# Kernel tuning notes

Hardware: AMD Instinct MI355X
Metric: run time of the kernel (lower is better)

Reference implementation:

```python
import jax, jax.numpy as jnp
import numpy as np

N, E, IN_DIM, C = 30000, 300000, 128, 16


def _xavier(key, shape):
    fan_in, fan_out = shape[1], shape[0]
    lim = np.sqrt(6.0 / (fan_in + fan_out))
    return jax.random.uniform(key, shape, jnp.float32, -lim, lim)


def layernorm(x, g, b, eps=1e-5):
    mu = jnp.mean(x, axis=-1, keepdims=True)
    var = jnp.var(x, axis=-1, keepdims=True)
    return (x - mu) * jax.lax.rsqrt(var + eps) * g + b


def setup_inputs() -> dict:
    key = jax.random.key(0)
    ks = jax.random.split(key, 8)
    D9 = C * 9            # 144
    DI = C * (C * 2)      # 512
    return {
        "x": jax.random.normal(ks[0], (N, IN_DIM), jnp.float32),
        "h": jax.random.normal(ks[1], (N, IN_DIM), jnp.float32),
        "local_frames": jax.random.normal(ks[2], (N, 3, 3), jnp.float32),
        "edge_index": jax.random.randint(ks[3], (2, E), 0, N, jnp.int64),
        "batch": jnp.zeros((N,), jnp.int64),
        # tensor_init: Linear(IN_DIM,144) LN SiLU Linear(144,144) LN SiLU
        "W1": _xavier(ks[4], (D9, IN_DIM)), "b1": jnp.zeros((D9,), jnp.float32),
        "g1": jnp.ones((D9,), jnp.float32), "be1": jnp.zeros((D9,), jnp.float32),
        "W2": _xavier(ks[5], (D9, D9)), "b2": jnp.zeros((D9,), jnp.float32),
        "g2": jnp.ones((D9,), jnp.float32), "be2": jnp.zeros((D9,), jnp.float32),
        # tensor_interaction: Linear(2*IN_DIM,512) LN Sigmoid
        "Wi": _xavier(ks[6], (DI, 2 * IN_DIM)), "bi": jnp.zeros((DI,), jnp.float32),
        "gi": jnp.ones((DI,), jnp.float32), "bei": jnp.zeros((DI,), jnp.float32),
    }


def reference(x, h, local_frames, edge_index, batch,
              W1, b1, g1, be1, W2, b2, g2, be2, Wi, bi, gi, bei):
    n = x.shape[0]
    row, col = edge_index[0], edge_index[1]

    # tensor_init(h) -> [N, C, 3, 3]
    t = jax.nn.silu(layernorm(h @ W1.T + b1, g1, be1))
    t = jax.nn.silu(layernorm(t @ W2.T + b2, g2, be2))
    tensors = t.reshape(n, C, 3, 3)

    hi, hj = h[col], h[row]
    ti, tj = tensors[col], tensors[row]
    Ri, Rj = local_frames[col], local_frames[row]

    # R_rel = Ri^T @ Rj : [E,3,3]
    R_rel = jnp.einsum('eki,ekj->eij', Ri, Rj)
    # rotate sender tensor: R_rel T R_rel^T
    tj_in_i = jnp.einsum('eik,eckl,elj->ecij', R_rel, tj, R_rel)

    stacked_tensor = jnp.concatenate([ti, tj_in_i], axis=1)          # [E,2C,3,3]
    stacked_scalars = jnp.concatenate([hi, hj], axis=-1)             # [E,2*IN_DIM]
    w = jax.nn.sigmoid(layernorm(stacked_scalars @ Wi.T + bi, gi, bei))
    int_weights = w.reshape(-1, 2 * C, C)                            # [E,2C,C]

    t_new = jnp.einsum('ekij,ekc->ecij', stacked_tensor, int_weights)  # [E,C,3,3]

    t_out = jax.ops.segment_sum(t_new, col, num_segments=n)           # [N,C,3,3]
    t_out = 0.5 * (t_out + jnp.swapaxes(t_out, -1, -2))
    return t_out
```

## Files before the change

kernel.cpp:

```cpp
#include <hip/hip_runtime.h>

#define NN 30000
#define EE 300000
#define HD 128
#define D9 144

typedef unsigned int uint32;
typedef unsigned short u16;
typedef __attribute__((ext_vector_type(8))) short short8;
typedef __attribute__((ext_vector_type(4))) float f32x4;
typedef __attribute__((ext_vector_type(4))) uint32 u32x4;

__device__ __forceinline__ float sigmoidf_(float x){ return __builtin_amdgcn_rcpf(1.0f + __expf(-x)); }
__device__ __forceinline__ float siluf_(float x){ return x * __builtin_amdgcn_rcpf(1.0f + __expf(-x)); }
__device__ __forceinline__ u16 f2bf(float f){
  uint32 u = __float_as_uint(f);
  return (u16)((u + 0x7fffu + ((u>>16)&1u)) >> 16);
}
__device__ __forceinline__ float bf2f(u16 b){ return __uint_as_float(((uint32)b)<<16); }
__device__ __forceinline__ float bflo(uint32 u){ return __uint_as_float(u<<16); }
__device__ __forceinline__ float bfhi(uint32 u){ return __uint_as_float(u & 0xffff0000u); }
__device__ __forceinline__ uint32 pk2(float a, float b){ return (uint32)f2bf(a) | ((uint32)f2bf(b)<<16); }

__global__ __launch_bounds__(256) void cvt_all_k(
    const float* __restrict__ Wi, u16* __restrict__ Wq,
    const float* __restrict__ W1, u16* __restrict__ W1s,
    const float* __restrict__ W2, u16* __restrict__ W2s,
    const float* __restrict__ gi, const float* __restrict__ bei,
    float* __restrict__ gt, float* __restrict__ bet)
{
  int i = blockIdx.x*256 + threadIdx.x;
  if (i < 512*128){
    int n = i >> 7, k = i & 127;
    float xl = Wi[n*256 + k];
    float xr = Wi[n*256 + 128 + k];
    u16 lh = f2bf(xl);
    Wq[i]          = lh;
    Wq[65536 + i]  = f2bf(xl - bf2f(lh));
    u16 rh = f2bf(xr);
    Wq[131072 + i] = rh;
    Wq[196608 + i] = f2bf(xr - bf2f(rh));
  }
  if (i < 144*128){
    float x = W1[i];
    u16 hh = f2bf(x);
    W1s[i] = hh;
    W1s[18432 + i] = f2bf(x - bf2f(hh));
  }
  if (i < 144*160){
    int r = i / 160, k = i - r*160;
    float x = (k < 144) ? W2[r*144 + k] : 0.f;
    u16 hh = f2bf(x);
    W2s[i] = hh;
    W2s[23040 + i] = f2bf(x - bf2f(hh));
  }
  if (i < 512){
    int c = i & 15, k = i >> 4;
    gt [c*32 + k] = gi[i];
    bet[c*32 + k] = bei[i];
  }
}

__global__ __launch_bounds__(256) void hist_k(const int* __restrict__ ei, uint32* __restrict__ start){
  int e = blockIdx.x*256 + threadIdx.x;
  if (e < EE){
    int col = ei[EE + e];
    col = col < 0 ? 0 : (col >= NN ? NN-1 : col);
    atomicAdd(&start[col], 1u);
  }
}

__global__ __launch_bounds__(1024) void scan_k(uint32* __restrict__ start){
  __shared__ uint32 part[1024];
  const int t = threadIdx.x;
  const int base = t * 30;
  uint32 loc[30];
  uint32 s = 0;
  #pragma unroll
  for (int i = 0; i < 30; ++i){
    int idx = base + i;
    uint32 cv = (idx < NN) ? start[idx] : 0u;
    loc[i] = s;
    s += cv;
  }
  part[t] = s;
  __syncthreads();
  for (int off = 1; off < 1024; off <<= 1){
    uint32 add = (t >= off) ? part[t - off] : 0u;
    __syncthreads();
    part[t] += add;
    __syncthreads();
  }
  uint32 pre = (t == 0) ? 0u : part[t - 1];
  #pragma unroll
  for (int i = 0; i < 30; ++i){
    int idx = base + i;
    if (idx < NN) start[idx] = pre + loc[i];
  }
}

__global__ __launch_bounds__(256) void scatter_k(const int* __restrict__ ei,
                                                 uint32* __restrict__ start,
                                                 u16* __restrict__ srow, u16* __restrict__ scol){
  int e = blockIdx.x*256 + threadIdx.x;
  if (e < EE){
    int row = ei[e];
    row = row < 0 ? 0 : (row >= NN ? NN-1 : row);
    int col = ei[EE + e];
    col = col < 0 ? 0 : (col >= NN ? NN-1 : col);
    uint32 pos = atomicAdd(&start[col], 1u);
    srow[pos] = (u16)row;
    scol[pos] = (u16)col;
  }
}

__global__ __launch_bounds__(256) void node_all_k(
    const float* __restrict__ h, const u16* __restrict__ Wq,
    const float* __restrict__ bi,
    const u16* __restrict__ W1s, const u16* __restrict__ W2s,
    const float* __restrict__ b1, const float* __restrict__ g1, const float* __restrict__ be1,
    const float* __restrict__ b2, const float* __restrict__ g2, const float* __restrict__ be2,
    u16* __restrict__ uu_t, u16* __restrict__ v16_t, float* __restrict__ tens_t)
{
  __shared__ float t1s[16 * 164];
  __shared__ float pool[160];

  const int t = threadIdx.x;
  const int w = t >> 6, l = t & 63, lr = l & 15, lg = l >> 4;
  const int nb = blockIdx.x * 16;
  const int ntile = (w == 0) ? 3 : 2;
  int tiles[3]; tiles[0] = 2*w; tiles[1] = 2*w + 1; tiles[2] = 8;

  short8 aH[4], aL[4];
  {
    const float* qA = h + (size_t)(nb + lr) * HD + lg*8;
    #pragma unroll
    for (int ks = 0; ks < 4; ++ks){
      float4 x0 = *(const float4*)(qA + ks*32);
      float4 x1 = *(const float4*)(qA + ks*32 + 4);
      float xs[8] = {x0.x, x0.y, x0.z, x0.w, x1.x, x1.y, x1.z, x1.w};
      #pragma unroll
      for (int j = 0; j < 8; ++j){
        u16 hh = f2bf(xs[j]);
        aH[ks][j] = (short)hh;
        aL[ks][j] = (short)f2bf(xs[j] - bf2f(hh));
      }
    }
  }

  {
    f32x4 au[8], av[8];
    #pragma unroll
    for (int nt = 0; nt < 8; ++nt){ au[nt] = (f32x4){0,0,0,0}; av[nt] = (f32x4){0,0,0,0}; }
    #pragma unroll
    for (int ks = 0; ks < 4; ++ks){
      #pragma unroll
      for (int nt = 0; nt < 8; ++nt){
        const u16* bu = Wq + (w*128 + nt*16 + lr)*128 + lg*8 + ks*32;
        short8 bH = *(const short8*)bu;
        short8 bL = *(const short8*)(bu + 65536);
        au[nt] = __builtin_amdgcn_mfma_f32_16x16x32_bf16(aH[ks], bH, au[nt], 0, 0, 0);
        au[nt] = __builtin_amdgcn_mfma_f32_16x16x32_bf16(aL[ks], bH, au[nt], 0, 0, 0);
        au[nt] = __builtin_amdgcn_mfma_f32_16x16x32_bf16(aH[ks], bL, au[nt], 0, 0, 0);
        const u16* bv = bu + 131072;
        short8 cH = *(const short8*)bv;
        short8 cL = *(const short8*)(bv + 65536);
        av[nt] = __builtin_amdgcn_mfma_f32_16x16x32_bf16(aH[ks], cH, av[nt], 0, 0, 0);
        av[nt] = __builtin_amdgcn_mfma_f32_16x16x32_bf16(aL[ks], cH, av[nt], 0, 0, 0);
        av[nt] = __builtin_amdgcn_mfma_f32_16x16x32_bf16(aH[ks], cL, av[nt], 0, 0, 0);
      }
    }
    float bb[8];
    #pragma unroll
    for (int nt = 0; nt < 8; ++nt) bb[nt] = bi[w*128 + nt*16 + lr];
    #pragma unroll
    for (int r = 0; r < 4; ++r){
      size_t node = nb + lg*4 + r;
      u32x4 pu;
      pu.x = pk2(au[0][r]+bb[0], au[1][r]+bb[1]);
      pu.y = pk2(au[2][r]+bb[2], au[3][r]+bb[3]);
      pu.z = pk2(au[4][r]+bb[4], au[5][r]+bb[5]);
      pu.w = pk2(au[6][r]+bb[6], au[7][r]+bb[7]);
      *(u32x4*)(uu_t + node*512 + lr*32 + w*8) = pu;
      u32x4 pv;
      pv.x = pk2(av[0][r], av[1][r]); pv.y = pk2(av[2][r], av[3][r]);
      pv.z = pk2(av[4][r], av[5][r]); pv.w = pk2(av[6][r], av[7][r]);
      *(u32x4*)(v16_t + node*512 + lr*32 + w*8) = pv;
    }
  }

  f32x4 acc[3];
  #pragma unroll
  for (int ti = 0; ti < 3; ++ti) acc[ti] = (f32x4){0,0,0,0};
  #pragma unroll
  for (int ks = 0; ks < 4; ++ks){
    for (int ti = 0; ti < ntile; ++ti){
      const u16* b = W1s + (tiles[ti]*16 + lr)*128 + lg*8 + ks*32;
      short8 bH = *(const short8*)b;
      short8 bL = *(const short8*)(b + 18432);
      acc[ti] = __builtin_amdgcn_mfma_f32_16x16x32_bf16(aH[ks], bH, acc[ti], 0, 0, 0);
      acc[ti] = __builtin_amdgcn_mfma_f32_16x16x32_bf16(aL[ks], bH, acc[ti], 0, 0, 0);
      acc[ti] = __builtin_amdgcn_mfma_f32_16x16x32_bf16(aH[ks], bL, acc[ti], 0, 0, 0);
    }
  }
  for (int ti = 0; ti < ntile; ++ti){
    float bb = b1[tiles[ti]*16 + lr];
    #pragma unroll
    for (int r = 0; r < 4; ++r) acc[ti][r] += bb;
  }
  {
    float ps[4], pq[4];
    #pragma unroll
    for (int r = 0; r < 4; ++r){
      float s = 0.f, q = 0.f;
      for (int ti = 0; ti < ntile; ++ti){ s += acc[ti][r]; q += acc[ti][r]*acc[ti][r]; }
      ps[r] = s; pq[r] = q;
    }
    #pragma unroll
    for (int off = 1; off < 16; off <<= 1)
      #pragma unroll
      for (int r = 0; r < 4; ++r){ ps[r] += __shfl_xor(ps[r], off); pq[r] += __shfl_xor(pq[r], off); }
    if (lr == 0){
      #pragma unroll
      for (int r = 0; r < 4; ++r){
        pool[w*32 + (lg*4 + r)*2 + 0] = ps[r];
        pool[w*32 + (lg*4 + r)*2 + 1] = pq[r];
      }
    }
  }
  __syncthreads();
  if (t < 16){
    float s = pool[t*2] + pool[32 + t*2] + pool[64 + t*2] + pool[96 + t*2];
    float q = pool[t*2+1] + pool[32 + t*2+1] + pool[64 + t*2+1] + pool[96 + t*2+1];
    float mu = s * (1.0f/144.0f);
    pool[128 + t] = mu;
    pool[144 + t] = rsqrtf(q * (1.0f/144.0f) - mu*mu + 1e-5f);
  }
  __syncthreads();
  for (int ti = 0; ti < ntile; ++ti){
    int col = tiles[ti]*16 + lr;
    float gg = g1[col], bb = be1[col];
    #pragma unroll
    for (int r = 0; r < 4; ++r){
      int node = lg*4 + r;
      float mu = pool[128 + node], rs = pool[144 + node];
      t1s[node*164 + col] = siluf_((acc[ti][r] - mu) * rs * gg + bb);
    }
  }
  t1s[(t >> 4)*164 + 144 + (t & 15)] = 0.f;
  __syncthreads();

  #pragma unroll
  for (int ti = 0; ti < 3; ++ti) acc[ti] = (f32x4){0,0,0,0};
  #pragma unroll
  for (int ks = 0; ks < 5; ++ks){
    float4 x0 = *(const float4*)&t1s[lr*164 + lg*8 + ks*32];
    float4 x1 = *(const float4*)&t1s[lr*164 + lg*8 + ks*32 + 4];
    float xs[8] = {x0.x, x0.y, x0.z, x0.w, x1.x, x1.y, x1.z, x1.w};
    short8 a2H, a2L;
    #pragma unroll
    for (int j = 0; j < 8; ++j){
      u16 hh = f2bf(xs[j]);
      a2H[j] = (short)hh;
      a2L[j] = (short)f2bf(xs[j] - bf2f(hh));
    }
    for (int ti = 0; ti < ntile; ++ti){
      const u16* b = W2s + (tiles[ti]*16 + lr)*160 + lg*8 + ks*32;
      short8 bH = *(const short8*)b;
      short8 bL = *(const short8*)(b + 23040);
      acc[ti] = __builtin_amdgcn_mfma_f32_16x16x32_bf16(a2H, bH, acc[ti], 0, 0, 0);
      acc[ti] = __builtin_amdgcn_mfma_f32_16x16x32_bf16(a2L, bH, acc[ti], 0, 0, 0);
      acc[ti] = __builtin_amdgcn_mfma_f32_16x16x32_bf16(a2H, bL, acc[ti], 0, 0, 0);
    }
  }
  for (int ti = 0; ti < ntile; ++ti){
    float bb = b2[tiles[ti]*16 + lr];
    #pragma unroll
    for (int r = 0; r < 4; ++r) acc[ti][r] += bb;
  }
  __syncthreads();
  {
    float ps[4], pq[4];
    #pragma unroll
    for (int r = 0; r < 4; ++r){
      float s = 0.f, q = 0.f;
      for (int ti = 0; ti < ntile; ++ti){ s += acc[ti][r]; q += acc[ti][r]*acc[ti][r]; }
      ps[r] = s; pq[r] = q;
    }
    #pragma unroll
    for (int off = 1; off < 16; off <<= 1)
      #pragma unroll
      for (int r = 0; r < 4; ++r){ ps[r] += __shfl_xor(ps[r], off); pq[r] += __shfl_xor(pq[r], off); }
    if (lr == 0){
      #pragma unroll
      for (int r = 0; r < 4; ++r){
        pool[w*32 + (lg*4 + r)*2 + 0] = ps[r];
        pool[w*32 + (lg*4 + r)*2 + 1] = pq[r];
      }
    }
  }
  __syncthreads();
  if (t < 16){
    float s = pool[t*2] + pool[32 + t*2] + pool[64 + t*2] + pool[96 + t*2];
    float q = pool[t*2+1] + pool[32 + t*2+1] + pool[64 + t*2+1] + pool[96 + t*2+1];
    float mu = s * (1.0f/144.0f);
    pool[128 + t] = mu;
    pool[144 + t] = rsqrtf(q * (1.0f/144.0f) - mu*mu + 1e-5f);
  }
  __syncthreads();
  for (int ti = 0; ti < ntile; ++ti){
    int col = tiles[ti]*16 + lr;
    float gg = g2[col], bb = be2[col];
    int c = col / 9, m = col - c*9;
    #pragma unroll
    for (int r = 0; r < 4; ++r){
      int node = lg*4 + r;
      float mu = pool[128 + node], rs = pool[144 + node];
      float val = siluf_((acc[ti][r] - mu) * rs * gg + bb);
      tens_t[(size_t)(nb + node)*144 + m*16 + c] = val;
    }
  }
}

__global__ __launch_bounds__(256) void edge_par_k(
    const u16* __restrict__ uu_t, const u16* __restrict__ v16_t,
    const float* __restrict__ frames, const float* __restrict__ tens_t,
    const float* __restrict__ gt, const float* __restrict__ bet,
    const u16* __restrict__ srow, const u16* __restrict__ scol,
    uint32* __restrict__ tn)
{
  const int t  = threadIdx.x;
  const int le = t >> 5;
  const int hf = (t >> 4) & 1;
  const int c  = t & 15;
  const int e  = blockIdx.x*8 + le;
  const int row = (int)srow[e], col = (int)scol[e];

  float z[16];
  {
    const u16* up = uu_t  + (size_t)col*512 + c*32 + hf*16;
    const u16* vp = v16_t + (size_t)row*512 + c*32 + hf*16;
    #pragma unroll
    for (int q = 0; q < 2; ++q){
      u32x4 ua = *(const u32x4*)(up + q*8);
      u32x4 va = *(const u32x4*)(vp + q*8);
      z[q*8+0] = bflo(ua.x)+bflo(va.x); z[q*8+1] = bfhi(ua.x)+bfhi(va.x);
      z[q*8+2] = bflo(ua.y)+bflo(va.y); z[q*8+3] = bfhi(ua.y)+bfhi(va.y);
      z[q*8+4] = bflo(ua.z)+bflo(va.z); z[q*8+5] = bfhi(ua.z)+bfhi(va.z);
      z[q*8+6] = bflo(ua.w)+bflo(va.w); z[q*8+7] = bfhi(ua.w)+bfhi(va.w);
    }
  }

  float s = 0.f, q2 = 0.f;
  #pragma unroll
  for (int k = 0; k < 16; ++k){ s += z[k]; q2 += z[k]*z[k]; }
  #pragma unroll
  for (int off = 1; off < 32; off <<= 1){ s += __shfl_xor(s, off); q2 += __shfl_xor(q2, off); }
  float mu = s * (1.0f/512.0f);
  float rs = rsqrtf(q2 * (1.0f/512.0f) - mu*mu + 1e-5f);

  {
    const float* gp = gt  + c*32 + hf*16;
    const float* bp = bet + c*32 + hf*16;
    #pragma unroll
    for (int kq = 0; kq < 4; ++kq){
      float4 g4 = *(const float4*)(gp + kq*4);
      float4 b4 = *(const float4*)(bp + kq*4);
      z[kq*4+0] = sigmoidf_((z[kq*4+0]-mu)*rs*g4.x + b4.x);
      z[kq*4+1] = sigmoidf_((z[kq*4+1]-mu)*rs*g4.y + b4.y);
      z[kq*4+2] = sigmoidf_((z[kq*4+2]-mu)*rs*g4.z + b4.z);
      z[kq*4+3] = sigmoidf_((z[kq*4+3]-mu)*rs*g4.w + b4.w);
    }
  }

  float P[9];
  {
    const float* T = tens_t + (size_t)(hf ? row : col) * 144;
    #pragma unroll
    for (int m = 0; m < 9; ++m){
      float4 a0 = *(const float4*)(T + m*16);
      float4 a1 = *(const float4*)(T + m*16 + 4);
      float4 a2 = *(const float4*)(T + m*16 + 8);
      float4 a3 = *(const float4*)(T + m*16 + 12);
      P[m] = a0.x*z[0]  + a0.y*z[1]  + a0.z*z[2]  + a0.w*z[3]
           + a1.x*z[4]  + a1.y*z[5]  + a1.z*z[6]  + a1.w*z[7]
           + a2.x*z[8]  + a2.y*z[9]  + a2.z*z[10] + a2.w*z[11]
           + a3.x*z[12] + a3.y*z[13] + a3.z*z[14] + a3.w*z[15];
    }
  }

  if (hf){
    const float* Ri = frames + (size_t)col*9;
    const float* Rj = frames + (size_t)row*9;
    float R[9];
    #pragma unroll
    for (int i = 0; i < 3; ++i)
      #pragma unroll
      for (int j = 0; j < 3; ++j)
        R[i*3+j] = Ri[i]*Rj[j] + Ri[3+i]*Rj[3+j] + Ri[6+i]*Rj[6+j];
    float A[9];
    #pragma unroll
    for (int i = 0; i < 3; ++i)
      #pragma unroll
      for (int j = 0; j < 3; ++j)
        A[i*3+j] = R[i*3+0]*P[0+j] + R[i*3+1]*P[3+j] + R[i*3+2]*P[6+j];
    #pragma unroll
    for (int i = 0; i < 3; ++i)
      #pragma unroll
      for (int j = 0; j < 3; ++j)
        P[i*3+j] = A[i*3+0]*R[0+j] + A[i*3+1]*R[3+j] + A[i*3+2]*R[6+j];
  }

  #pragma unroll
  for (int m = 0; m < 9; ++m) P[m] += __shfl_xor(P[m], 16);

  if (hf == 0){
    float s01 = 0.5f*(P[1]+P[3]), s02 = 0.5f*(P[2]+P[6]), s12 = 0.5f*(P[5]+P[7]);
    uint32* tp = tn + (size_t)e*48 + c*3;
    __builtin_nontemporal_store(pk2(P[0], s01), tp + 0);
    __builtin_nontemporal_store(pk2(s02, P[4]), tp + 1);
    __builtin_nontemporal_store(pk2(s12, P[8]), tp + 2);
  }
}

__global__ __launch_bounds__(256) void segsum_k(
    const uint32* __restrict__ tn, const uint32* __restrict__ start,
    float* __restrict__ out)
{
  int tid = blockIdx.x*256 + threadIdx.x;
  if (tid >= NN*16) return;
  int n = tid >> 4, c = tid & 15;
  uint32 beg = (n == 0) ? 0u : start[n-1];
  uint32 end = start[n];

  float a0=0.f, a1=0.f, a2=0.f, a3=0.f, a4=0.f, a5=0.f;
  for (uint32 i = beg; i < end; ++i){
    const uint32* tp = tn + (size_t)i*48 + c*3;
    uint32 x0 = __builtin_nontemporal_load(tp + 0);
    uint32 x1 = __builtin_nontemporal_load(tp + 1);
    uint32 x2 = __builtin_nontemporal_load(tp + 2);
    a0 += bflo(x0); a1 += bfhi(x0);
    a2 += bflo(x1); a3 += bfhi(x1);
    a4 += bflo(x2); a5 += bfhi(x2);
  }

  float* op = out + (size_t)n*144 + c*9;
  __builtin_nontemporal_store(a0, op + 0);
  __builtin_nontemporal_store(a1, op + 1);
  __builtin_nontemporal_store(a2, op + 2);
  __builtin_nontemporal_store(a1, op + 3);
  __builtin_nontemporal_store(a3, op + 4);
  __builtin_nontemporal_store(a4, op + 5);
  __builtin_nontemporal_store(a2, op + 6);
  __builtin_nontemporal_store(a4, op + 7);
  __builtin_nontemporal_store(a5, op + 8);
}

extern "C" void kernel_launch(void* const* d_in, const int* in_sizes, int n_in,
                              void* d_out, int out_size, void* d_ws, size_t ws_size,
                              hipStream_t stream) {
    const float* h      = (const float*)d_in[1];
    const float* frames = (const float*)d_in[2];
    const int*   ei     = (const int*)d_in[3];
    const float* W1  = (const float*)d_in[5];
    const float* b1  = (const float*)d_in[6];
    const float* g1  = (const float*)d_in[7];
    const float* be1 = (const float*)d_in[8];
    const float* W2  = (const float*)d_in[9];
    const float* b2  = (const float*)d_in[10];
    const float* g2  = (const float*)d_in[11];
    const float* be2 = (const float*)d_in[12];
    const float* Wi  = (const float*)d_in[13];
    const float* bi  = (const float*)d_in[14];
    const float* gi  = (const float*)d_in[15];
    const float* bei = (const float*)d_in[16];

    float* out = (float*)d_out;

    u16*    uu_t  = (u16*)d_ws;
    u16*    v16_t = (u16*)  ((char*)d_ws + 30720000);
    float*  tens_t= (float*)((char*)d_ws + 61440000);
    u16*    Wq    = (u16*)  ((char*)d_ws + 78720000);
    u16*    W1s   = (u16*)  ((char*)d_ws + 79244288);
    u16*    W2s   = (u16*)  ((char*)d_ws + 79318016);
    float*  gt    = (float*)((char*)d_ws + 79410176);
    float*  bet   = (float*)((char*)d_ws + 79412224);
    uint32* start = (uint32*)((char*)d_ws + 79414272);
    u16*    srow  = (u16*)  ((char*)d_ws + 79534272);
    u16*    scol  = (u16*)  ((char*)d_ws + 80134272);
    uint32* tn    = (uint32*)((char*)d_ws + 80734272);

    hipMemsetAsync(start, 0, NN * sizeof(uint32), stream);

    cvt_all_k<<<256, 256, 0, stream>>>(Wi, Wq, W1, W1s, W2, W2s, gi, bei, gt, bet);
    node_all_k<<<NN/16, 256, 0, stream>>>(h, Wq, bi, W1s, W2s, b1, g1, be1, b2, g2, be2,
                                          uu_t, v16_t, tens_t);
    hist_k<<<(EE + 255)/256, 256, 0, stream>>>(ei, start);
    scan_k<<<1, 1024, 0, stream>>>(start);
    scatter_k<<<(EE + 255)/256, 256, 0, stream>>>(ei, start, srow, scol);
    edge_par_k<<<EE/8, 256, 0, stream>>>(uu_t, v16_t, frames, tens_t, gt, bet, srow, scol, tn);
    segsum_k<<<(NN*16 + 255)/256, 256, 0, stream>>>(tn, start, out);
}
```

Measured before the change: 618.4 us.

## Fold histogram into weight-conversion kernel, add nontemporal stores, unroll segsum loop

The edge histogram (atomicAdd per edge) moves into the weight-conversion kernel, which now launches enough blocks to cover all edges, so one kernel launch is removed. The node kernel's uu/v16/tensor outputs become nontemporal stores, meant to reduce cache pollution since edge_par_k reads them later in a gather pattern. The segmented-sum loop is unrolled by two so more loads are in flight per iteration. Risks: nontemporal stores may evict data that edge_par_k would otherwise find in L2, and the conversion kernel now runs many blocks that do only the histogram work.

```diff
diff --git a/kernel.cpp b/kernel.cpp
--- a/kernel.cpp
+++ b/kernel.cpp
@@ -27,7 +27,8 @@
     const float* __restrict__ W1, u16* __restrict__ W1s,
     const float* __restrict__ W2, u16* __restrict__ W2s,
     const float* __restrict__ gi, const float* __restrict__ bei,
-    float* __restrict__ gt, float* __restrict__ bet)
+    float* __restrict__ gt, float* __restrict__ bet,
+    const int* __restrict__ ei, uint32* __restrict__ start)
 {
   int i = blockIdx.x*256 + threadIdx.x;
   if (i < 512*128){
@@ -59,12 +60,8 @@
     gt [c*32 + k] = gi[i];
     bet[c*32 + k] = bei[i];
   }
-}
-
-__global__ __launch_bounds__(256) void hist_k(const int* __restrict__ ei, uint32* __restrict__ start){
-  int e = blockIdx.x*256 + threadIdx.x;
-  if (e < EE){
-    int col = ei[EE + e];
+  if (i < EE){
+    int col = ei[EE + i];
     col = col < 0 ? 0 : (col >= NN ? NN-1 : col);
     atomicAdd(&start[col], 1u);
   }
@@ -181,11 +178,11 @@
       pu.y = pk2(au[2][r]+bb[2], au[3][r]+bb[3]);
       pu.z = pk2(au[4][r]+bb[4], au[5][r]+bb[5]);
       pu.w = pk2(au[6][r]+bb[6], au[7][r]+bb[7]);
-      *(u32x4*)(uu_t + node*512 + lr*32 + w*8) = pu;
+      __builtin_nontemporal_store(pu, (u32x4*)(uu_t + node*512 + lr*32 + w*8));
       u32x4 pv;
       pv.x = pk2(av[0][r], av[1][r]); pv.y = pk2(av[2][r], av[3][r]);
       pv.z = pk2(av[4][r], av[5][r]); pv.w = pk2(av[6][r], av[7][r]);
-      *(u32x4*)(v16_t + node*512 + lr*32 + w*8) = pv;
+      __builtin_nontemporal_store(pv, (u32x4*)(v16_t + node*512 + lr*32 + w*8));
     }
   }
 
@@ -317,7 +314,7 @@
       int node = lg*4 + r;
       float mu = pool[128 + node], rs = pool[144 + node];
       float val = siluf_((acc[ti][r] - mu) * rs * gg + bb);
-      tens_t[(size_t)(nb + node)*144 + m*16 + c] = val;
+      __builtin_nontemporal_store(val, tens_t + (size_t)(nb + node)*144 + m*16 + c);
     }
   }
 }
@@ -434,7 +431,21 @@
   uint32 end = start[n];
 
   float a0=0.f, a1=0.f, a2=0.f, a3=0.f, a4=0.f, a5=0.f;
-  for (uint32 i = beg; i < end; ++i){
+  uint32 i = beg;
+  for (; i + 2 <= end; i += 2){
+    const uint32* tp0 = tn + (size_t)i*48 + c*3;
+    const uint32* tp1 = tn + (size_t)(i+1)*48 + c*3;
+    uint32 x0 = __builtin_nontemporal_load(tp0 + 0);
+    uint32 x1 = __builtin_nontemporal_load(tp0 + 1);
+    uint32 x2 = __builtin_nontemporal_load(tp0 + 2);
+    uint32 y0 = __builtin_nontemporal_load(tp1 + 0);
+    uint32 y1 = __builtin_nontemporal_load(tp1 + 1);
+    uint32 y2 = __builtin_nontemporal_load(tp1 + 2);
+    a0 += bflo(x0) + bflo(y0); a1 += bfhi(x0) + bfhi(y0);
+    a2 += bflo(x1) + bflo(y1); a3 += bfhi(x1) + bfhi(y1);
+    a4 += bflo(x2) + bflo(y2); a5 += bfhi(x2) + bfhi(y2);
+  }
+  if (i < end){
     const uint32* tp = tn + (size_t)i*48 + c*3;
     uint32 x0 = __builtin_nontemporal_load(tp + 0);
     uint32 x1 = __builtin_nontemporal_load(tp + 1);
@@ -492,10 +503,10 @@
 
     hipMemsetAsync(start, 0, NN * sizeof(uint32), stream);
 
-    cvt_all_k<<<256, 256, 0, stream>>>(Wi, Wq, W1, W1s, W2, W2s, gi, bei, gt, bet);
+    cvt_all_k<<<(EE + 255)/256, 256, 0, stream>>>(Wi, Wq, W1, W1s, W2, W2s, gi, bei, gt, bet,
+                                                  ei, start);
     node_all_k<<<NN/16, 256, 0, stream>>>(h, Wq, bi, W1s, W2s, b1, g1, be1, b2, g2, be2,
                                           uu_t, v16_t, tens_t);
-    hist_k<<<(EE + 255)/256, 256, 0, stream>>>(ei, start);
     scan_k<<<1, 1024, 0, stream>>>(start);
     scatter_k<<<(EE + 255)/256, 256, 0, stream>>>(ei, start, srow, scol);
     edge_par_k<<<EE/8, 256, 0, stream>>>(uu_t, v16_t, frames, tens_t, gt, bet, srow, scol, tn);
```

New measurement: 650.1 us. 5.1% more time.
